# Performance work log

Measured on AMD Instinct MI355X. Metric: run time of the kernel, lower is better.

Reference implementation:

```python
import jax, jax.numpy as jnp
import numpy as np
from jax import lax

B, L = 8, 1024
C_IN, D_MODEL = 3, 512
N_MAMBA, N_TRANS, NHEAD = 2, 2, 8
D_STATE, D_CONV, EXPAND = 16, 4, 2
DI = EXPAND * D_MODEL            # 1024, mamba inner dim
DT_RANK = D_MODEL // 16          # 32
DH = D_MODEL // NHEAD            # 64, head dim
DFF = 4 * D_MODEL


def setup_inputs() -> dict:
    key = jax.random.key(0)
    ks = iter(jax.random.split(key, 64))
    def rn(shape, s=0.05):
        return jax.random.normal(next(ks), shape, jnp.float32) * s
    inp = {
        'x': jax.random.normal(next(ks), (B, C_IN, L), jnp.float32),
        'proj_w': rn((D_MODEL, C_IN)), 'proj_b': rn((D_MODEL,)),
        # stacked per-mamba-layer params (leading dim = N_MAMBA)
        'm_in_w': rn((N_MAMBA, 2 * DI, D_MODEL)),
        'm_conv_w': rn((N_MAMBA, DI, D_CONV)), 'm_conv_b': rn((N_MAMBA, DI)),
        'm_xproj_w': rn((N_MAMBA, DT_RANK + 2 * D_STATE, DI)),
        'm_dt_w': rn((N_MAMBA, DI, DT_RANK)), 'm_dt_b': rn((N_MAMBA, DI)),
        'm_Alog': jnp.tile(jnp.log(jnp.arange(1, D_STATE + 1, dtype=jnp.float32)), (N_MAMBA, DI, 1)),
        'm_D': jnp.ones((N_MAMBA, DI), jnp.float32),
        'm_out_w': rn((N_MAMBA, D_MODEL, DI)),
        'm_ln_w': jnp.ones((N_MAMBA, D_MODEL), jnp.float32), 'm_ln_b': jnp.zeros((N_MAMBA, D_MODEL), jnp.float32),
        # stacked per-transformer-layer params
        't_qkv_w': rn((N_TRANS, 3 * D_MODEL, D_MODEL)), 't_qkv_b': rn((N_TRANS, 3 * D_MODEL)),
        't_ow': rn((N_TRANS, D_MODEL, D_MODEL)), 't_ob': rn((N_TRANS, D_MODEL)),
        't_l1w': rn((N_TRANS, DFF, D_MODEL)), 't_l1b': rn((N_TRANS, DFF)),
        't_l2w': rn((N_TRANS, D_MODEL, DFF)), 't_l2b': rn((N_TRANS, D_MODEL)),
        't_ln1w': jnp.ones((N_TRANS, D_MODEL), jnp.float32), 't_ln1b': jnp.zeros((N_TRANS, D_MODEL), jnp.float32),
        't_ln2w': jnp.ones((N_TRANS, D_MODEL), jnp.float32), 't_ln2b': jnp.zeros((N_TRANS, D_MODEL), jnp.float32),
        'no_w': jnp.ones((D_MODEL,), jnp.float32), 'no_b': jnp.zeros((D_MODEL,), jnp.float32),
    }
    return inp


def _ln(x, w, b, eps=1e-5):
    m = x.mean(-1, keepdims=True)
    v = ((x - m) ** 2).mean(-1, keepdims=True)
    return (x - m) / jnp.sqrt(v + eps) * w + b


def _pos_encoding(length, d):
    pos = jnp.arange(length, dtype=jnp.float32)[:, None]
    div = jnp.exp(jnp.arange(0, d, 2, dtype=jnp.float32) * (-np.log(10000.0) / d))
    pe = jnp.zeros((length, d), jnp.float32)
    pe = pe.at[:, 0::2].set(jnp.sin(pos * div)).at[:, 1::2].set(jnp.cos(pos * div))
    return pe


def _mamba(h, in_w, conv_w, conv_b, xp_w, dt_w, dt_b, Alog, Dp, out_w):
    # h: [B,L,d_model]
    xz = h @ in_w.T                                   # [B,L,2*DI]
    xm, z = jnp.split(xz, 2, axis=-1)
    # causal depthwise conv1d over time
    k = conv_w.T[:, None, :]                          # [D_CONV,1,DI]
    xc = lax.conv_general_dilated(xm, k, (1,), [(D_CONV - 1, 0)],
                                  dimension_numbers=('NWC', 'WIO', 'NWC'),
                                  feature_group_count=DI) + conv_b
    xc = jax.nn.silu(xc)
    xdb = xc @ xp_w.T                                 # [B,L,DT_RANK+2*D_STATE]
    dt = jax.nn.softplus(xdb[..., :DT_RANK] @ dt_w.T + dt_b)   # [B,L,DI]
    Bm = xdb[..., DT_RANK:DT_RANK + D_STATE]          # [B,L,D_STATE]
    Cm = xdb[..., DT_RANK + D_STATE:]                 # [B,L,D_STATE]
    A = -jnp.exp(Alog)                                # [DI,D_STATE]

    def step(state, t):
        dt_t, B_t, C_t, x_t = t                       # [B,DI],[B,S],[B,S],[B,DI]
        dA = jnp.exp(dt_t[..., None] * A)             # [B,DI,S]
        state = state * dA + (dt_t * x_t)[..., None] * B_t[:, None, :]
        y = jnp.einsum('bds,bs->bd', state, C_t)
        return state, y

    init = jnp.zeros((h.shape[0], DI, D_STATE), h.dtype)
    seq = (dt.transpose(1, 0, 2), Bm.transpose(1, 0, 2), Cm.transpose(1, 0, 2), xc.transpose(1, 0, 2))
    _, ys = lax.scan(step, init, seq)                 # ys: [L,B,DI]
    y = ys.transpose(1, 0, 2) + Dp * xc
    y = y * jax.nn.silu(z)
    return y @ out_w.T                                # [B,L,d_model]


def _transformer_layer(h, qkv_w, qkv_b, ow, ob, l1w, l1b, l2w, l2b, ln1w, ln1b, ln2w, ln2b):
    Bt, Lt, d = h.shape
    qkv = h @ qkv_w.T + qkv_b
    q, k, v = jnp.split(qkv, 3, axis=-1)
    q = q.reshape(Bt, Lt, NHEAD, DH); k = k.reshape(Bt, Lt, NHEAD, DH); v = v.reshape(Bt, Lt, NHEAD, DH)
    sc = jnp.einsum('blhd,bmhd->bhlm', q, k) / np.sqrt(DH).astype(np.float32)
    a = jax.nn.softmax(sc, axis=-1)
    o = jnp.einsum('bhlm,bmhd->blhd', a, v).reshape(Bt, Lt, d)
    h = _ln(h + o @ ow.T + ob, ln1w, ln1b)
    ff = jax.nn.relu(h @ l1w.T + l1b) @ l2w.T + l2b
    return _ln(h + ff, ln2w, ln2b)


def reference(x, proj_w, proj_b, m_in_w, m_conv_w, m_conv_b, m_xproj_w, m_dt_w, m_dt_b,
              m_Alog, m_D, m_out_w, m_ln_w, m_ln_b, t_qkv_w, t_qkv_b, t_ow, t_ob,
              t_l1w, t_l1b, t_l2w, t_l2b, t_ln1w, t_ln1b, t_ln2w, t_ln2b, no_w, no_b):
    # proj_in: 1x1 conv == pointwise linear over channels; output [B,L,d]
    h = jnp.einsum('bcl,dc->bld', x, proj_w) + proj_b
    for i in range(N_MAMBA):
        h = _ln(h + _mamba(h, m_in_w[i], m_conv_w[i], m_conv_b[i], m_xproj_w[i],
                           m_dt_w[i], m_dt_b[i], m_Alog[i], m_D[i], m_out_w[i]),
                m_ln_w[i], m_ln_b[i])
    h = h + _pos_encoding(h.shape[1], D_MODEL)
    for i in range(N_TRANS):
        h = _transformer_layer(h, t_qkv_w[i], t_qkv_b[i], t_ow[i], t_ob[i],
                               t_l1w[i], t_l1b[i], t_l2w[i], t_l2b[i],
                               t_ln1w[i], t_ln1b[i], t_ln2w[i], t_ln2b[i])
    h = _ln(h, no_w, no_b)
    return h, h.mean(axis=1)
```

## Files before the change

### kernel.cpp

```cpp
#include <hip/hip_runtime.h>
#include <cstddef>

#define BATCH 8
#define LSEQ 1024
#define DMODEL 512
#define DINNER 1024
#define DSTATE 16
#define DTRANK 32
#define NHEAD 8
#define DHEAD 64
#define DFF 2048
#define MTOK 8192
#define NCHUNK 16
#define CLEN 64

typedef __attribute__((ext_vector_type(8))) short bfrag;
typedef __attribute__((ext_vector_type(4))) float f32x4;
typedef __attribute__((ext_vector_type(4))) unsigned short us4;
typedef unsigned short ushort_t;

__device__ __forceinline__ float silu_f(float x) { return x / (1.f + __expf(-x)); }

__device__ __forceinline__ unsigned short f2bf(float f) {
  unsigned u = __float_as_uint(f);
  return (unsigned short)((u + 0x7FFFu + ((u >> 16) & 1u)) >> 16);
}
__device__ __forceinline__ float bf2f(ushort_t u) {
  return __uint_as_float((unsigned)u << 16);
}

__device__ __forceinline__ void gll16(const ushort_t* g, ushort_t* l) {
  __builtin_amdgcn_global_load_lds(
      (const __attribute__((address_space(1))) unsigned int*)g,
      (__attribute__((address_space(3))) unsigned int*)l, 16, 0, 0);
}

struct Cvt8Args {
  const float* s[8];
  ushort_t* d[8];
  int end[8];
};
__global__ __launch_bounds__(256) void cvt8(Cvt8Args a) {
  int blk = blockIdx.x;
  int seg = 0, start = 0;
#pragma unroll
  for (int i = 0; i < 7; ++i)
    if (blk >= a.end[i]) { seg = i + 1; start = a.end[i]; }
  int i4 = (blk - start) * 256 + threadIdx.x;
  float4 v = ((const float4*)a.s[seg])[i4];
  us4 o = {f2bf(v.x), f2bf(v.y), f2bf(v.z), f2bf(v.w)};
  ((us4*)a.d[seg])[i4] = o;
}

__global__ __launch_bounds__(256) void proj_kernel(const float* __restrict__ x,
                                                   const float* __restrict__ pw,
                                                   const float* __restrict__ pb,
                                                   float* __restrict__ h,
                                                   ushort_t* __restrict__ hbf) {
  int idx = blockIdx.x * 256 + threadIdx.x;
  int d = idx & 511;
  int l = (idx >> 9) & 1023;
  int b = idx >> 19;
  const float* xb = x + (size_t)b * 3 * 1024 + l;
  float v = pb[d] + xb[0] * pw[d * 3] + xb[1024] * pw[d * 3 + 1] + xb[2048] * pw[d * 3 + 2];
  h[idx] = v;
  hbf[idx] = f2bf(v);
}

template <int ACT, int CBF, int SPLITK, int BN>
__global__ __launch_bounds__(256) void gemm_gll(const ushort_t* __restrict__ A,
                                                const ushort_t* __restrict__ W,
                                                const float* __restrict__ bias,
                                                void* __restrict__ Cp,
                                                int K, int lda, int ldc) {
  __shared__ ushort_t sA[2][4096];
  __shared__ ushort_t sB[2][BN * 32];
  constexpr int MREP = (BN == 128) ? 4 : 2;
  const int bm = blockIdx.y * 128, bn = blockIdx.x * BN;
  const int tid = threadIdx.x;
  const int wid = tid >> 6, lane = tid & 63;
  const int wrb = (BN == 128) ? (wid >> 1) * 64 : wid * 32;
  const int wcb = (BN == 128) ? (wid & 1) * 64 : 0;
  const int lr = lane & 15, ls = lane >> 4;
  const int sw = ls ^ ((lr >> 1) & 3);

  const int kseg = K / SPLITK;
  const int kbeg = (SPLITK > 1) ? blockIdx.z * kseg : 0;

  const int c0 = wid * 128 + lane;
  const int c1 = c0 + 64;
  const int r0 = c0 >> 2, s0 = (c0 & 3) ^ ((r0 >> 1) & 3);
  const int r1 = c1 >> 2, s1 = (c1 & 3) ^ ((r1 >> 1) & 3);
  const ushort_t* gA0 = A + (size_t)(bm + r0) * lda + kbeg + s0 * 8;
  const ushort_t* gA1 = A + (size_t)(bm + r1) * lda + kbeg + s1 * 8;
  const ushort_t* gB0;
  const ushort_t* gB1 = nullptr;
  if constexpr (BN == 128) {
    gB0 = W + (size_t)(bn + r0) * K + kbeg + s0 * 8;
    gB1 = W + (size_t)(bn + r1) * K + kbeg + s1 * 8;
  } else {
    const int cb = wid * 64 + lane;
    const int rb = cb >> 2, sb2 = (cb & 3) ^ ((rb >> 1) & 3);
    gB0 = W + (size_t)(bn + rb) * K + kbeg + sb2 * 8;
  }

  f32x4 acc[MREP][4];
#pragma unroll
  for (int i = 0; i < MREP; ++i)
#pragma unroll
    for (int j = 0; j < 4; ++j) acc[i][j] = (f32x4)(0.f);

#define STAGE(buf, step)                                             \
  do {                                                               \
    gll16(gA0 + (step) * 32, &sA[buf][wid * 1024]);                  \
    gll16(gA1 + (step) * 32, &sA[buf][wid * 1024 + 512]);            \
    if constexpr (BN == 128) {                                       \
      gll16(gB0 + (step) * 32, &sB[buf][wid * 1024]);                \
      gll16(gB1 + (step) * 32, &sB[buf][wid * 1024 + 512]);          \
    } else {                                                         \
      gll16(gB0 + (step) * 32, &sB[buf][wid * 512]);                 \
    }                                                                \
  } while (0)

  const int NT = kseg / 32;
  STAGE(0, 0);
  for (int t = 0; t < NT; ++t) {
    const int cur = t & 1;
    if (t + 1 < NT) {
      STAGE(cur ^ 1, t + 1);
      if constexpr (BN == 128)
        asm volatile("s_waitcnt vmcnt(4)" ::: "memory");
      else
        asm volatile("s_waitcnt vmcnt(3)" ::: "memory");
    } else {
      asm volatile("s_waitcnt vmcnt(0)" ::: "memory");
    }
    __builtin_amdgcn_sched_barrier(0);
    __builtin_amdgcn_s_barrier();
    __builtin_amdgcn_sched_barrier(0);

    bfrag af[MREP], bf[4];
#pragma unroll
    for (int mi = 0; mi < MREP; ++mi) {
      int row = wrb + mi * 16 + lr;
      af[mi] = *(const bfrag*)&sA[cur][(size_t)((row << 2) + sw) * 8];
    }
#pragma unroll
    for (int nj = 0; nj < 4; ++nj) {
      int col = wcb + nj * 16 + lr;
      bf[nj] = *(const bfrag*)&sB[cur][(size_t)((col << 2) + sw) * 8];
    }
#pragma unroll
    for (int mi = 0; mi < MREP; ++mi)
#pragma unroll
      for (int nj = 0; nj < 4; ++nj)
        acc[mi][nj] = __builtin_amdgcn_mfma_f32_16x16x32_bf16(af[mi], bf[nj], acc[mi][nj], 0, 0, 0);

    __builtin_amdgcn_s_barrier();
    __builtin_amdgcn_sched_barrier(0);
  }
#undef STAGE

  if (SPLITK > 1) {
#pragma unroll
    for (int nj = 0; nj < 4; ++nj) {
      int col = bn + wcb + nj * 16 + lr;
#pragma unroll
      for (int mi = 0; mi < MREP; ++mi) {
        int row0 = bm + wrb + mi * 16 + ls * 4;
#pragma unroll
        for (int r = 0; r < 4; ++r) {
          if (CBF)
            ((ushort_t*)Cp)[(size_t)blockIdx.z * 8192 * ldc +
                            (size_t)(row0 + r) * ldc + col] = f2bf(acc[mi][nj][r]);
          else
            ((float*)Cp)[(size_t)blockIdx.z * 8192 * ldc +
                         (size_t)(row0 + r) * ldc + col] = acc[mi][nj][r];
        }
      }
    }
  } else {
#pragma unroll
    for (int nj = 0; nj < 4; ++nj) {
      int col = bn + wcb + nj * 16 + lr;
      float bv = bias ? bias[col] : 0.f;
#pragma unroll
      for (int mi = 0; mi < MREP; ++mi) {
        int row0 = bm + wrb + mi * 16 + ls * 4;
#pragma unroll
        for (int r = 0; r < 4; ++r) {
          float v = acc[mi][nj][r] + bv;
          if (ACT == 1) v = fmaxf(v, 0.f);
          if (ACT == 2) v = (v > 20.f) ? v : log1pf(__expf(v));
          if (CBF)
            ((ushort_t*)Cp)[(size_t)(row0 + r) * ldc + col] = f2bf(v);
          else
            ((float*)Cp)[(size_t)(row0 + r) * ldc + col] = v;
        }
      }
    }
  }
}

__global__ __launch_bounds__(256) void reduce8_xdb(const float* __restrict__ p,
                                                   float* __restrict__ xdb,
                                                   ushort_t* __restrict__ xdb_bf) {
  int i = blockIdx.x * 256 + threadIdx.x;
  float4 a = ((const float4*)p)[i];
#pragma unroll
  for (int z = 1; z < 8; ++z) {
    float4 b = ((const float4*)p)[i + z * 131072];
    a.x += b.x; a.y += b.y; a.z += b.z; a.w += b.w;
  }
  ((float4*)xdb)[i] = a;
  us4 o = {f2bf(a.x), f2bf(a.y), f2bf(a.z), f2bf(a.w)};
  ((us4*)xdb_bf)[i] = o;
}

__global__ __launch_bounds__(256) void conv_silu_kernel(const unsigned* __restrict__ xz,
                                                        const float* __restrict__ cw,
                                                        const float* __restrict__ cb,
                                                        unsigned* __restrict__ xc) {
  int idx = blockIdx.x * 256 + threadIdx.x;
  int dp = idx & 511;
  int t = (idx >> 9) & 1023;
  int b = idx >> 19;
  int d0 = dp * 2;
  float a0 = cb[d0], a1 = cb[d0 + 1];
#pragma unroll
  for (int w = 0; w < 4; ++w) {
    int tt = t - 3 + w;
    if (tt >= 0) {
      unsigned v = xz[(((size_t)(b * 1024 + tt)) << 10) + dp];
      a0 += bf2f((ushort_t)(v & 0xffff)) * cw[d0 * 4 + w];
      a1 += bf2f((ushort_t)(v >> 16)) * cw[(d0 + 1) * 4 + w];
    }
  }
  unsigned o = (unsigned)f2bf(silu_f(a0)) | ((unsigned)f2bf(silu_f(a1)) << 16);
  xc[(((size_t)(b * 1024 + t)) << 9) + dp] = o;
}

__global__ __launch_bounds__(256) void scan_pass1(const ushort_t* __restrict__ dt,
                                                  const float* __restrict__ xdb,
                                                  const ushort_t* __restrict__ xc,
                                                  const float* __restrict__ Alog,
                                                  float* __restrict__ scrP,
                                                  float* __restrict__ scrL) {
  int idx = blockIdx.x * 256 + threadIdx.x;
  int sh = idx & 3;
  int d = (idx >> 2) & 1023;
  int c = (idx >> 12) & 15;
  int b = idx >> 16;
  float A[4], st[4], P[4];
#pragma unroll
  for (int s = 0; s < 4; ++s) {
    A[s] = -__expf(Alog[d * 16 + sh * 4 + s]);
    st[s] = 0.f;
    P[s] = 1.f;
  }
  int t0 = c * CLEN;
  size_t base = (((size_t)(b * 1024 + t0)) << 10) + d;
  const float* xb = xdb + (size_t)(b * 1024 + t0) * 64 + 32 + sh * 4;
  float dtv = bf2f(dt[base]), xv = bf2f(xc[base]);
  for (int t = 0; t < CLEN; ++t) {
    float dtn = 0.f, xvn = 0.f;
    if (t + 1 < CLEN) { dtn = bf2f(dt[base + 1024]); xvn = bf2f(xc[base + 1024]); }
    float4 Bv = *(const float4*)xb;
    float dx = dtv * xv;
    float e0 = __expf(dtv * A[0]), e1 = __expf(dtv * A[1]);
    float e2 = __expf(dtv * A[2]), e3 = __expf(dtv * A[3]);
    st[0] = st[0] * e0 + dx * Bv.x; P[0] *= e0;
    st[1] = st[1] * e1 + dx * Bv.y; P[1] *= e1;
    st[2] = st[2] * e2 + dx * Bv.z; P[2] *= e2;
    st[3] = st[3] * e3 + dx * Bv.w; P[3] *= e3;
    base += 1024; xb += 64;
    dtv = dtn; xv = xvn;
  }
  size_t pbase = (((size_t)((b * 16 + c) * 16 + sh * 4)) << 10) + d;
#pragma unroll
  for (int s = 0; s < 4; ++s) {
    scrP[pbase + ((size_t)s << 10)] = P[s];
    scrL[pbase + ((size_t)s << 10)] = st[s];
  }
}

__global__ __launch_bounds__(256) void scan_pass2(const float* __restrict__ scrP,
                                                  float* __restrict__ scrL) {
  int idx = blockIdx.x * 256 + threadIdx.x;
  int d = idx & 1023;
  int s = (idx >> 10) & 15;
  int b = idx >> 14;
  float cur = 0.f;
  for (int c = 0; c < 16; ++c) {
    size_t o = (((size_t)(((b * 16 + c) * 16) + s)) << 10) + d;
    float P = scrP[o];
    float loc = scrL[o];
    scrL[o] = cur;
    cur = cur * P + loc;
  }
}

__global__ __launch_bounds__(256) void scan_pass3(const ushort_t* __restrict__ dt,
                                                  const float* __restrict__ xdb,
                                                  const ushort_t* __restrict__ xc,
                                                  const ushort_t* __restrict__ xz,
                                                  ushort_t* __restrict__ ybf,
                                                  const float* __restrict__ Alog,
                                                  const float* __restrict__ Dp,
                                                  const float* __restrict__ scrL) {
  int idx = blockIdx.x * 256 + threadIdx.x;
  int sh = idx & 3;
  int d = (idx >> 2) & 1023;
  int c = (idx >> 12) & 15;
  int b = idx >> 16;
  float A[4], st[4];
  size_t pbase = (((size_t)((b * 16 + c) * 16 + sh * 4)) << 10) + d;
#pragma unroll
  for (int s = 0; s < 4; ++s) {
    A[s] = -__expf(Alog[d * 16 + sh * 4 + s]);
    st[s] = scrL[pbase + ((size_t)s << 10)];
  }
  float Dv = Dp[d];
  int t0 = c * CLEN;
  size_t base = (((size_t)(b * 1024 + t0)) << 10) + d;
  size_t zoff = ((((size_t)(b * 1024 + t0)) << 11)) + 1024 + d;
  const float* xb = xdb + (size_t)(b * 1024 + t0) * 64 + 32 + sh * 4;
  float dtv = bf2f(dt[base]), xv = bf2f(xc[base]), zv = bf2f(xz[zoff]);
  for (int t = 0; t < CLEN; ++t) {
    float dtn = 0.f, xvn = 0.f, zvn = 0.f;
    if (t + 1 < CLEN) {
      dtn = bf2f(dt[base + 1024]); xvn = bf2f(xc[base + 1024]); zvn = bf2f(xz[zoff + 2048]);
    }
    float4 Bv = *(const float4*)xb;
    float4 Cv = *(const float4*)(xb + 16);
    float dx = dtv * xv;
    float e0 = __expf(dtv * A[0]), e1 = __expf(dtv * A[1]);
    float e2 = __expf(dtv * A[2]), e3 = __expf(dtv * A[3]);
    st[0] = st[0] * e0 + dx * Bv.x;
    st[1] = st[1] * e1 + dx * Bv.y;
    st[2] = st[2] * e2 + dx * Bv.z;
    st[3] = st[3] * e3 + dx * Bv.w;
    float acc = st[0] * Cv.x + st[1] * Cv.y + st[2] * Cv.z + st[3] * Cv.w;
    acc += __shfl_xor(acc, 1);
    acc += __shfl_xor(acc, 2);
    if (sh == 0)
      ybf[base] = f2bf((acc + Dv * xv) * silu_f(zv));
    base += 1024; zoff += 2048; xb += 64;
    dtv = dtn; xv = xvn; zv = zvn;
  }
}

__global__ __launch_bounds__(128) void resid_ln_kernel(const float* __restrict__ x,
                                                       const float* __restrict__ add,
                                                       const float* __restrict__ w,
                                                       const float* __restrict__ bias,
                                                       float* __restrict__ out,
                                                       ushort_t* __restrict__ out_bf) {
  int row = blockIdx.x, tid = threadIdx.x;
  float4 v = ((const float4*)(x + (size_t)row * 512))[tid];
  if (add) {
    float4 a = ((const float4*)(add + (size_t)row * 512))[tid];
    v.x += a.x; v.y += a.y; v.z += a.z; v.w += a.w;
  }
  float s = v.x + v.y + v.z + v.w;
  float ss = v.x * v.x + v.y * v.y + v.z * v.z + v.w * v.w;
#pragma unroll
  for (int o = 32; o; o >>= 1) {
    s += __shfl_xor(s, o);
    ss += __shfl_xor(ss, o);
  }
  __shared__ float red[4];
  int wid = tid >> 6;
  if ((tid & 63) == 0) { red[wid] = s; red[2 + wid] = ss; }
  __syncthreads();
  s = red[0] + red[1];
  ss = red[2] + red[3];
  float mean = s * (1.f / 512.f);
  float var = ss * (1.f / 512.f) - mean * mean;
  float inv = rsqrtf(var + 1e-5f);
  float4 wv = ((const float4*)w)[tid];
  float4 bv = ((const float4*)bias)[tid];
  float4 ov;
  ov.x = (v.x - mean) * inv * wv.x + bv.x;
  ov.y = (v.y - mean) * inv * wv.y + bv.y;
  ov.z = (v.z - mean) * inv * wv.z + bv.z;
  ov.w = (v.w - mean) * inv * wv.w + bv.w;
  ((float4*)(out + (size_t)row * 512))[tid] = ov;
  if (out_bf) {
    us4 ob = {f2bf(ov.x), f2bf(ov.y), f2bf(ov.z), f2bf(ov.w)};
    ((us4*)(out_bf + (size_t)row * 512))[tid] = ob;
  }
}

__global__ __launch_bounds__(128) void resid_ln_sk(const float* __restrict__ x,
                                                   const ushort_t* __restrict__ p,
                                                   const float* __restrict__ pbias,
                                                   const float* __restrict__ w,
                                                   const float* __restrict__ bias,
                                                   float* __restrict__ out,
                                                   ushort_t* __restrict__ out_bf) {
  int row = blockIdx.x, tid = threadIdx.x;
  float4 v = ((const float4*)(x + (size_t)row * 512))[tid];
  us4 a = ((const us4*)(p + (size_t)row * 512))[tid];
  us4 c = ((const us4*)(p + 4194304 + (size_t)row * 512))[tid];
  v.x += bf2f(a.x) + bf2f(c.x);
  v.y += bf2f(a.y) + bf2f(c.y);
  v.z += bf2f(a.z) + bf2f(c.z);
  v.w += bf2f(a.w) + bf2f(c.w);
  if (pbias) {
    float4 pb = ((const float4*)pbias)[tid];
    v.x += pb.x; v.y += pb.y; v.z += pb.z; v.w += pb.w;
  }
  float s = v.x + v.y + v.z + v.w;
  float ss = v.x * v.x + v.y * v.y + v.z * v.z + v.w * v.w;
#pragma unroll
  for (int o = 32; o; o >>= 1) {
    s += __shfl_xor(s, o);
    ss += __shfl_xor(ss, o);
  }
  __shared__ float red[4];
  int wid = tid >> 6;
  if ((tid & 63) == 0) { red[wid] = s; red[2 + wid] = ss; }
  __syncthreads();
  s = red[0] + red[1];
  ss = red[2] + red[3];
  float mean = s * (1.f / 512.f);
  float var = ss * (1.f / 512.f) - mean * mean;
  float inv = rsqrtf(var + 1e-5f);
  float4 wv = ((const float4*)w)[tid];
  float4 bv = ((const float4*)bias)[tid];
  float4 ov;
  ov.x = (v.x - mean) * inv * wv.x + bv.x;
  ov.y = (v.y - mean) * inv * wv.y + bv.y;
  ov.z = (v.z - mean) * inv * wv.z + bv.z;
  ov.w = (v.w - mean) * inv * wv.w + bv.w;
  ((float4*)(out + (size_t)row * 512))[tid] = ov;
  us4 ob = {f2bf(ov.x), f2bf(ov.y), f2bf(ov.z), f2bf(ov.w)};
  ((us4*)(out_bf + (size_t)row * 512))[tid] = ob;
}

__global__ __launch_bounds__(256) void posenc_kernel(float* __restrict__ h,
                                                     ushort_t* __restrict__ hbf) {
  int idx = blockIdx.x * 256 + threadIdx.x;
  int d = idx & 511;
  int l = (idx >> 9) & 1023;
  float freq = __expf(-(float)(d & ~1) * (9.210340371976184f / 512.f));
  float ang = (float)l * freq;
  float v = h[idx] + ((d & 1) ? cosf(ang) : sinf(ang));
  h[idx] = v;
  hbf[idx] = f2bf(v);
}

__global__ __launch_bounds__(256, 8) void attn_mfma(const ushort_t* __restrict__ qkv,
                                                    ushort_t* __restrict__ ao) {
  __shared__ unsigned short Qs[4096];
  __shared__ unsigned short Ks[4096];
  __shared__ unsigned short Vt[4096];
  __shared__ unsigned short Ps[4096];
  const int tid = threadIdx.x;
  const int w = blockIdx.x;
  const int bh = (w & 7) + (w >> 7) * 8;
  const int qt = (w >> 3) & 15;
  const int hh = bh & 7, b = bh >> 3;
  const int l0 = qt * 64;
  const size_t bb = (size_t)b * 1024 * 1536;

  const int srow = tid >> 2;
  const int sdb = (tid & 3) << 4;
  const int sc0 = sdb >> 3;

  {
    const ushort_t* qp = qkv + bb + (size_t)(l0 + srow) * 1536 + hh * 64 + sdb;
    *(bfrag*)&Qs[srow * 64 + ((sc0 ^ (srow & 7)) << 3)] = *(const bfrag*)qp;
    *(bfrag*)&Qs[srow * 64 + (((sc0 + 1) ^ (srow & 7)) << 3)] = *(const bfrag*)(qp + 8);
  }

  const int wid = tid >> 6, lane = tid & 63;
  const int l15 = lane & 15, rg = lane >> 4;
  const int l7 = l15 & 7;
  float m[4], lsum[4];
  f32x4 oacc[4];
#pragma unroll
  for (int r = 0; r < 4; ++r) { m[r] = -1e30f; lsum[r] = 0.f; }
#pragma unroll
  for (int nt = 0; nt < 4; ++nt) oacc[nt] = (f32x4)(0.f);

  for (int jt = 0; jt < 16; ++jt) {
    {
      const ushort_t* kp = qkv + bb + (size_t)(jt * 64 + srow) * 1536 + hh * 64 + 512 + sdb;
      *(bfrag*)&Ks[srow * 64 + ((sc0 ^ (srow & 7)) << 3)] = *(const bfrag*)kp;
      *(bfrag*)&Ks[srow * 64 + (((sc0 + 1) ^ (srow & 7)) << 3)] = *(const bfrag*)(kp + 8);
      const ushort_t* vp = kp + 512;
      unsigned short vv[16];
      *(bfrag*)&vv[0] = *(const bfrag*)vp;
      *(bfrag*)&vv[8] = *(const bfrag*)(vp + 8);
#pragma unroll
      for (int j = 0; j < 16; ++j) {
        int dd = sdb + j;
        Vt[dd * 64 + (((srow >> 3) ^ (dd & 7) ^ ((dd >> 3) & 7)) << 3) + (srow & 7)] = vv[j];
      }
    }
    __syncthreads();

    bfrag aq[2];
#pragma unroll
    for (int ks = 0; ks < 2; ++ks)
      aq[ks] = *(const bfrag*)&Qs[(wid * 16 + l15) * 64 + (((ks * 4 + rg) ^ l7) << 3)];
    f32x4 sc[4];
#pragma unroll
    for (int nt = 0; nt < 4; ++nt) {
      f32x4 s = (f32x4)(0.f);
#pragma unroll
      for (int ks = 0; ks < 2; ++ks) {
        bfrag bk = *(const bfrag*)&Ks[(nt * 16 + l15) * 64 + (((ks * 4 + rg) ^ l7) << 3)];
        s = __builtin_amdgcn_mfma_f32_16x16x32_bf16(aq[ks], bk, s, 0, 0, 0);
      }
      sc[nt] = s * 0.125f;
    }

#pragma unroll
    for (int r = 0; r < 4; ++r) {
      float mc = fmaxf(fmaxf(sc[0][r], sc[1][r]), fmaxf(sc[2][r], sc[3][r]));
#pragma unroll
      for (int o = 8; o; o >>= 1) mc = fmaxf(mc, __shfl_xor(mc, o));
      float mn = fmaxf(m[r], mc);
      float al = __expf(m[r] - mn);
      m[r] = mn;
      int prow = rg * 4 + r;
      float ps = 0.f;
#pragma unroll
      for (int nt = 0; nt < 4; ++nt) {
        float p = __expf(sc[nt][r] - mn);
        ps += p;
        int col = nt * 16 + l15;
        Ps[wid * 1024 + prow * 64 + ((((col >> 3) ^ (prow & 7))) << 3) + (col & 7)] =
            (ushort_t)(__float_as_uint(p) >> 16);
      }
#pragma unroll
      for (int o = 8; o; o >>= 1) ps += __shfl_xor(ps, o);
      lsum[r] = lsum[r] * al + ps;
#pragma unroll
      for (int nt = 0; nt < 4; ++nt) oacc[nt][r] *= al;
    }

    bfrag ap[2];
#pragma unroll
    for (int ks = 0; ks < 2; ++ks)
      ap[ks] = *(const bfrag*)&Ps[wid * 1024 + l15 * 64 + (((ks * 4 + rg) ^ l7) << 3)];
#pragma unroll
    for (int nt = 0; nt < 4; ++nt) {
      int vrow = nt * 16 + l15;
#pragma unroll
      for (int ks = 0; ks < 2; ++ks) {
        bfrag bv = *(const bfrag*)&Vt[vrow * 64 +
            (((ks * 4 + rg) ^ (vrow & 7) ^ ((vrow >> 3) & 7)) << 3)];
        oacc[nt] = __builtin_amdgcn_mfma_f32_16x16x32_bf16(ap[ks], bv, oacc[nt], 0, 0, 0);
      }
    }
    __syncthreads();
  }

#pragma unroll
  for (int r = 0; r < 4; ++r) {
    float inv = 1.f / lsum[r];
    int row = l0 + wid * 16 + rg * 4 + r;
    ushort_t* op = ao + ((size_t)(b * 1024 + row)) * 512 + hh * 64;
#pragma unroll
    for (int nt = 0; nt < 4; ++nt) op[nt * 16 + l15] = f2bf(oacc[nt][r] * inv);
  }
}

__global__ __launch_bounds__(512) void mean_part(const float* __restrict__ h,
                                                 float* __restrict__ part) {
  int blk = blockIdx.x;
  int b = blk >> 4, lc = blk & 15, d = threadIdx.x;
  float s = 0.f;
  int l0 = lc * 64;
  for (int l = l0; l < l0 + 64; ++l) s += h[(((size_t)(b * 1024 + l)) << 9) + d];
  part[((size_t)blk << 9) + d] = s;
}
__global__ __launch_bounds__(256) void mean_final(const float* __restrict__ part,
                                                  float* __restrict__ out2) {
  int i = blockIdx.x * 256 + threadIdx.x;
  int b = i >> 9, d = i & 511;
  float s = 0.f;
#pragma unroll
  for (int c = 0; c < 16; ++c) s += part[(((size_t)(b * 16 + c)) << 9) + d];
  out2[i] = s * (1.f / 1024.f);
}

extern "C" void kernel_launch(void* const* d_in, const int* in_sizes, int n_in,
                              void* d_out, int out_size, void* d_ws, size_t ws_size,
                              hipStream_t stream) {
  const float* x        = (const float*)d_in[0];
  const float* proj_w   = (const float*)d_in[1];
  const float* proj_b   = (const float*)d_in[2];
  const float* m_in_w   = (const float*)d_in[3];
  const float* m_conv_w = (const float*)d_in[4];
  const float* m_conv_b = (const float*)d_in[5];
  const float* m_xproj_w= (const float*)d_in[6];
  const float* m_dt_w   = (const float*)d_in[7];
  const float* m_dt_b   = (const float*)d_in[8];
  const float* m_Alog   = (const float*)d_in[9];
  const float* m_D      = (const float*)d_in[10];
  const float* m_out_w  = (const float*)d_in[11];
  const float* m_ln_w   = (const float*)d_in[12];
  const float* m_ln_b   = (const float*)d_in[13];
  const float* t_qkv_w  = (const float*)d_in[14];
  const float* t_qkv_b  = (const float*)d_in[15];
  const float* t_ow     = (const float*)d_in[16];
  const float* t_ob     = (const float*)d_in[17];
  const float* t_l1w    = (const float*)d_in[18];
  const float* t_l1b    = (const float*)d_in[19];
  const float* t_l2w    = (const float*)d_in[20];
  const float* t_l2b    = (const float*)d_in[21];
  const float* t_ln1w   = (const float*)d_in[22];
  const float* t_ln1b   = (const float*)d_in[23];
  const float* t_ln2w   = (const float*)d_in[24];
  const float* t_ln2b   = (const float*)d_in[25];
  const float* no_w     = (const float*)d_in[26];
  const float* no_b     = (const float*)d_in[27];

  float* ws   = (float*)d_ws;
  float* h    = ws;
  ushort_t* h_bf = (ushort_t*)(ws + 4194304);
  float* bufA = ws + 6291456;
  float* bufB = bufA + 16777216;
  float* bufC = bufB + 8388608;
  float* bufE = bufC + 8388608;
  float* bufF = bufE + 4194304;
  ushort_t* y_bf = (ushort_t*)(bufF + 524288);
  ushort_t* wbf  = (ushort_t*)(bufF + 524288 + 4194304);
  float* scrP = bufE;
  float* scrL = bufE + 2097152;

  ushort_t* wIN  = wbf;
  ushort_t* wOUT = wbf + 2097152;
  ushort_t* wQKV = wbf + 3145728;
  ushort_t* wOW  = wbf + 4718592;
  ushort_t* wL1  = wbf + 5242880;
  ushort_t* wL2  = wbf + 7340032;
  ushort_t* wXP  = wbf + 9437184;
  ushort_t* wDT  = wbf + 9568256;
  ushort_t* xdb_bf = wbf + 9633792;

  Cvt8Args ca;
  ca.s[0] = m_in_w;    ca.d[0] = wIN;
  ca.s[1] = m_out_w;   ca.d[1] = wOUT;
  ca.s[2] = t_qkv_w;   ca.d[2] = wQKV;
  ca.s[3] = t_ow;      ca.d[3] = wOW;
  ca.s[4] = t_l1w;     ca.d[4] = wL1;
  ca.s[5] = t_l2w;     ca.d[5] = wL2;
  ca.s[6] = m_xproj_w; ca.d[6] = wXP;
  ca.s[7] = m_dt_w;    ca.d[7] = wDT;
  ca.end[0] = 2048; ca.end[1] = 3072; ca.end[2] = 4608; ca.end[3] = 5120;
  ca.end[4] = 7168; ca.end[5] = 9216; ca.end[6] = 9344; ca.end[7] = 9408;
  cvt8<<<9408, 256, 0, stream>>>(ca);

  proj_kernel<<<16384, 256, 0, stream>>>(x, proj_w, proj_b, h, h_bf);

  for (int i = 0; i < 2; ++i) {
    gemm_gll<0, 1, 1, 128><<<dim3(16, 64), 256, 0, stream>>>(
        h_bf, wIN + (size_t)i * 1048576, nullptr, bufA, DMODEL, DMODEL, 2 * DINNER);
    conv_silu_kernel<<<16384, 256, 0, stream>>>((const unsigned*)bufA,
                                                m_conv_w + i * DINNER * 4,
                                                m_conv_b + i * DINNER, (unsigned*)bufB);
    gemm_gll<0, 0, 8, 64><<<dim3(1, 64, 8), 256, 0, stream>>>(
        (const ushort_t*)bufB, wXP + (size_t)i * 65536, nullptr, bufC,
        DINNER, DINNER, 64);
    reduce8_xdb<<<512, 256, 0, stream>>>(bufC, bufF, xdb_bf);
    gemm_gll<2, 1, 1, 128><<<dim3(8, 64), 256, 0, stream>>>(
        xdb_bf, wDT + (size_t)i * 32768, m_dt_b + i * DINNER, bufC,
        DTRANK, 64, DINNER);
    scan_pass1<<<2048, 256, 0, stream>>>((const ushort_t*)bufC, bufF, (const ushort_t*)bufB,
                                         m_Alog + (size_t)i * DINNER * DSTATE, scrP, scrL);
    scan_pass2<<<512, 256, 0, stream>>>(scrP, scrL);
    scan_pass3<<<2048, 256, 0, stream>>>((const ushort_t*)bufC, bufF, (const ushort_t*)bufB,
                                         (const ushort_t*)bufA, y_bf,
                                         m_Alog + (size_t)i * DINNER * DSTATE,
                                         m_D + i * DINNER, scrL);
    gemm_gll<0, 1, 2, 128><<<dim3(4, 64, 2), 256, 0, stream>>>(
        y_bf, wOUT + (size_t)i * 524288, nullptr, bufC, DINNER, DINNER, DMODEL);
    resid_ln_sk<<<8192, 128, 0, stream>>>(h, (const ushort_t*)bufC, nullptr,
                                          m_ln_w + i * DMODEL, m_ln_b + i * DMODEL, h, h_bf);
  }

  posenc_kernel<<<16384, 256, 0, stream>>>(h, h_bf);

  for (int i = 0; i < 2; ++i) {
    gemm_gll<0, 1, 1, 128><<<dim3(12, 64), 256, 0, stream>>>(
        h_bf, wQKV + (size_t)i * 786432, t_qkv_b + i * 3 * DMODEL, bufA,
        DMODEL, DMODEL, 3 * DMODEL);
    attn_mfma<<<1024, 256, 0, stream>>>((const ushort_t*)bufA, (ushort_t*)bufB);
    gemm_gll<0, 1, 2, 128><<<dim3(4, 64, 2), 256, 0, stream>>>(
        (const ushort_t*)bufB, wOW + (size_t)i * 262144, nullptr, bufC,
        DMODEL, DMODEL, DMODEL);
    resid_ln_sk<<<8192, 128, 0, stream>>>(h, (const ushort_t*)bufC, t_ob + i * DMODEL,
                                          t_ln1w + i * DMODEL, t_ln1b + i * DMODEL, h, h_bf);
    gemm_gll<1, 1, 1, 128><<<dim3(16, 64), 256, 0, stream>>>(
        h_bf, wL1 + (size_t)i * 1048576, t_l1b + i * DFF, bufA,
        DMODEL, DMODEL, DFF);
    gemm_gll<0, 1, 2, 128><<<dim3(4, 64, 2), 256, 0, stream>>>(
        (const ushort_t*)bufA, wL2 + (size_t)i * 1048576, nullptr, bufC,
        DFF, DFF, DMODEL);
    resid_ln_sk<<<8192, 128, 0, stream>>>(h, (const ushort_t*)bufC, t_l2b + i * DMODEL,
                                          t_ln2w + i * DMODEL, t_ln2b + i * DMODEL, h, h_bf);
  }

  float* out_h = (float*)d_out;
  resid_ln_kernel<<<8192, 128, 0, stream>>>(h, nullptr, no_w, no_b, out_h, nullptr);
  mean_part<<<128, 512, 0, stream>>>(out_h, bufF);
  mean_final<<<16, 256, 0, stream>>>(bufF, out_h + 4194304);
}
```

Measured before the change: 947.8 us.

## Prefetch next K/V tile into registers in attention and simplify scan decay product

The attention kernel now loads the next K/V tile from global memory into registers while the current tile is being computed, and moves the barrier to the top of the loop. The occupancy hint drops from 8 to 5 waves so the extra registers fit. In scan_pass1 the per-step running product of decay factors is replaced by summing dt and taking one exponential at the end, which removes four multiplies per step. The changes aim to hide global-load latency in attention and trim ALU work in the scan, at the cost of higher register pressure and possibly lower occupancy.

```diff
diff --git a/kernel.cpp b/kernel.cpp
--- a/kernel.cpp
+++ b/kernel.cpp
@@ -251,13 +251,13 @@
   int d = (idx >> 2) & 1023;
   int c = (idx >> 12) & 15;
   int b = idx >> 16;
-  float A[4], st[4], P[4];
+  float A[4], st[4];
 #pragma unroll
   for (int s = 0; s < 4; ++s) {
     A[s] = -__expf(Alog[d * 16 + sh * 4 + s]);
     st[s] = 0.f;
-    P[s] = 1.f;
-  }
+  }
+  float dtsum = 0.f;
   int t0 = c * CLEN;
   size_t base = (((size_t)(b * 1024 + t0)) << 10) + d;
   const float* xb = xdb + (size_t)(b * 1024 + t0) * 64 + 32 + sh * 4;
@@ -269,17 +269,18 @@
     float dx = dtv * xv;
     float e0 = __expf(dtv * A[0]), e1 = __expf(dtv * A[1]);
     float e2 = __expf(dtv * A[2]), e3 = __expf(dtv * A[3]);
-    st[0] = st[0] * e0 + dx * Bv.x; P[0] *= e0;
-    st[1] = st[1] * e1 + dx * Bv.y; P[1] *= e1;
-    st[2] = st[2] * e2 + dx * Bv.z; P[2] *= e2;
-    st[3] = st[3] * e3 + dx * Bv.w; P[3] *= e3;
+    st[0] = st[0] * e0 + dx * Bv.x;
+    st[1] = st[1] * e1 + dx * Bv.y;
+    st[2] = st[2] * e2 + dx * Bv.z;
+    st[3] = st[3] * e3 + dx * Bv.w;
+    dtsum += dtv;
     base += 1024; xb += 64;
     dtv = dtn; xv = xvn;
   }
   size_t pbase = (((size_t)((b * 16 + c) * 16 + sh * 4)) << 10) + d;
 #pragma unroll
   for (int s = 0; s < 4; ++s) {
-    scrP[pbase + ((size_t)s << 10)] = P[s];
+    scrP[pbase + ((size_t)s << 10)] = __expf(A[s] * dtsum);
     scrL[pbase + ((size_t)s << 10)] = st[s];
   }
 }
@@ -451,7 +452,7 @@
   hbf[idx] = f2bf(v);
 }
 
-__global__ __launch_bounds__(256, 8) void attn_mfma(const ushort_t* __restrict__ qkv,
+__global__ __launch_bounds__(256, 5) void attn_mfma(const ushort_t* __restrict__ qkv,
                                                     ushort_t* __restrict__ ao) {
   __shared__ unsigned short Qs[4096];
   __shared__ unsigned short Ks[4096];
@@ -475,6 +476,17 @@
     *(bfrag*)&Qs[srow * 64 + (((sc0 + 1) ^ (srow & 7)) << 3)] = *(const bfrag*)(qp + 8);
   }
 
+  union B8 { bfrag v; ushort_t u[8]; };
+  bfrag k0, k1;
+  B8 v0, v1;
+  {
+    const ushort_t* kp = qkv + bb + (size_t)srow * 1536 + hh * 64 + 512 + sdb;
+    k0 = *(const bfrag*)kp;
+    k1 = *(const bfrag*)(kp + 8);
+    v0.v = *(const bfrag*)(kp + 512);
+    v1.v = *(const bfrag*)(kp + 520);
+  }
+
   const int wid = tid >> 6, lane = tid & 63;
   const int l15 = lane & 15, rg = lane >> 4;
   const int l7 = l15 & 7;
@@ -486,19 +498,21 @@
   for (int nt = 0; nt < 4; ++nt) oacc[nt] = (f32x4)(0.f);
 
   for (int jt = 0; jt < 16; ++jt) {
-    {
-      const ushort_t* kp = qkv + bb + (size_t)(jt * 64 + srow) * 1536 + hh * 64 + 512 + sdb;
-      *(bfrag*)&Ks[srow * 64 + ((sc0 ^ (srow & 7)) << 3)] = *(const bfrag*)kp;
-      *(bfrag*)&Ks[srow * 64 + (((sc0 + 1) ^ (srow & 7)) << 3)] = *(const bfrag*)(kp + 8);
-      const ushort_t* vp = kp + 512;
-      unsigned short vv[16];
-      *(bfrag*)&vv[0] = *(const bfrag*)vp;
-      *(bfrag*)&vv[8] = *(const bfrag*)(vp + 8);
-#pragma unroll
-      for (int j = 0; j < 16; ++j) {
-        int dd = sdb + j;
-        Vt[dd * 64 + (((srow >> 3) ^ (dd & 7) ^ ((dd >> 3) & 7)) << 3) + (srow & 7)] = vv[j];
-      }
+    __syncthreads();
+    *(bfrag*)&Ks[srow * 64 + ((sc0 ^ (srow & 7)) << 3)] = k0;
+    *(bfrag*)&Ks[srow * 64 + (((sc0 + 1) ^ (srow & 7)) << 3)] = k1;
+#pragma unroll
+    for (int j = 0; j < 16; ++j) {
+      int dd = sdb + j;
+      ushort_t val = (j < 8) ? v0.u[j] : v1.u[j - 8];
+      Vt[dd * 64 + (((srow >> 3) ^ (dd & 7) ^ ((dd >> 3) & 7)) << 3) + (srow & 7)] = val;
+    }
+    if (jt + 1 < 16) {
+      const ushort_t* kp = qkv + bb + (size_t)((jt + 1) * 64 + srow) * 1536 + hh * 64 + 512 + sdb;
+      k0 = *(const bfrag*)kp;
+      k1 = *(const bfrag*)(kp + 8);
+      v0.v = *(const bfrag*)(kp + 512);
+      v1.v = *(const bfrag*)(kp + 520);
     }
     __syncthreads();
 
@@ -557,7 +571,6 @@
         oacc[nt] = __builtin_amdgcn_mfma_f32_16x16x32_bf16(ap[ks], bv, oacc[nt], 0, 0, 0);
       }
     }
-    __syncthreads();
   }
 
 #pragma unroll
```

New measurement: 1.136 ms. 19.9% more time.
